# Performance work log

Hardware: AMD Instinct MI355X
Metric: run time of the kernel (lower is better)

Reference implementation:

```python
import jax, jax.numpy as jnp
import numpy as np

ALPHA = 0.2   # LeakyReLU negative slope
RATIO = 0.5   # blend ratio between attention and structural similarity
KHOP = 3      # k-hop structural similarity depth
NEG_BIG = -9e15


def _build_adj(edge, n):
    # edge: [N, D] int neighbor indices; adj[i, edge[i, d]] = 1
    rows = jnp.broadcast_to(jnp.arange(n)[:, None], edge.shape)
    return jnp.zeros((n, n), jnp.float32).at[rows, edge].set(1.0)


def _structural_similarity(adj, khop):
    # Sum of adjacency powers A + A^2 + ... + A^khop (k-hop reachability counts).
    s = adj
    p = adj
    for _ in range(khop - 1):
        p = p @ adj
        s = s + p
    return s


def _per_graph(atom, edge, W, a):
    n = atom.shape[0]
    adj = _build_adj(edge, n)
    structure = jax.nn.softmax(_structural_similarity(adj, KHOP), axis=1)
    h = atom @ W                                   # [N, F]
    f = h.shape[1]
    # a_input[i,j] = concat(h_i, h_j); a_input @ a == (h @ a1)_i + (h @ a2)_j
    src = h @ a[:f, 0]                             # [N]
    dst = h @ a[f:, 0]                             # [N]
    e = jax.nn.leaky_relu(src[:, None] + dst[None, :], ALPHA)  # [N, N]
    att = jnp.where(adj > 0, e, NEG_BIG)
    att = jax.nn.softmax(att, axis=1)
    blended = RATIO * att + (1.0 - RATIO) * structure
    return jax.nn.elu(blended @ h)                 # [N, F]


def setup_inputs() -> dict:
    key = jax.random.key(0)
    k1, k2, k3, k4 = jax.random.split(key, 4)
    B, N, D, F_IN, F_OUT = 16, 1024, 8, 128, 64
    atoms = jax.random.normal(k1, (B, N, F_IN), dtype=jnp.float32)
    edges = jax.random.randint(k2, (B, N, D), 0, N, dtype=jnp.int64)
    W = jax.random.normal(k3, (F_IN, F_OUT), dtype=jnp.float32) * 0.1
    a = jax.random.normal(k4, (2 * F_OUT, 1), dtype=jnp.float32) * 0.1
    return {"atoms": atoms, "edges": edges, "W": W, "a": a}


def reference(atoms, edges, W, a):
    return jax.vmap(_per_graph, in_axes=(0, 0, None, None))(atoms, edges, W, a)
```

## Files before the change

kernel.cpp:

```cpp
#include <hip/hip_runtime.h>

#define NN 1024
#define DG 8
#define FO 64
#define FI 128
#define LALPHA 0.2f
#define BR 16
#define SBS 257
#define MTS 1032

typedef __attribute__((ext_vector_type(8))) short bf16x8;
typedef __attribute__((ext_vector_type(4))) float f32x4;

static __device__ __forceinline__ unsigned short f2bf(float x) {
  union { float f; unsigned u; } v; v.f = x;
  unsigned r = v.u + 0x7FFFu + ((v.u >> 16) & 1u);
  return (unsigned short)(r >> 16);
}
static __device__ __forceinline__ float bf2f(unsigned short h) {
  union { unsigned u; float f; } v; v.u = ((unsigned)h) << 16;
  return v.f;
}

__global__ __launch_bounds__(256) void k_prep(const float* __restrict__ atoms,
                                              const float* __restrict__ W,
                                              const float* __restrict__ a,
                                              const int* __restrict__ edges,
                                              int* __restrict__ uniq,
                                              ushort* __restrict__ hT,
                                              float* __restrict__ srcv,
                                              float* __restrict__ dstv) {
  __shared__ float sp[16], dp[16];
  const int t = threadIdx.x, b = blockIdx.x;
  const int g = b >> 6;
  const int rbase = b * 16;

  if (t < 16) {
    sp[t] = 0.f; dp[t] = 0.f;
    const int rr = rbase + t;
    int e[DG];
#pragma unroll
    for (int s = 0; s < DG; s++) e[s] = edges[rr * DG + s];
#pragma unroll
    for (int s = 0; s < DG; s++) {
      int v = e[s];
      bool dup = false;
#pragma unroll
      for (int q = 0; q < DG; q++)
        if (q < s && e[q] == v) dup = true;
      uniq[rr * DG + s] = dup ? -1 : v;
    }
  }

  const int w = t >> 6, lane = t & 63, quad = lane >> 4, l16 = lane & 15;
  const float* __restrict__ Ar = atoms + (size_t)(rbase + l16) * FI;
  const float* __restrict__ Wc = W + w * 16 + l16;
  f32x4 acc = {0.f, 0.f, 0.f, 0.f};
#pragma unroll
  for (int kc = 0; kc < 4; kc++) {
    const int k0 = kc * 32 + quad * 8;
    float4 a0 = *(const float4*)(Ar + k0);
    float4 a1 = *(const float4*)(Ar + k0 + 4);
    float av[8] = {a0.x, a0.y, a0.z, a0.w, a1.x, a1.y, a1.z, a1.w};
    float wv[8];
#pragma unroll
    for (int e = 0; e < 8; e++) wv[e] = Wc[(k0 + e) * FO];
    bf16x8 ahi, alo, bhi, blo;
#pragma unroll
    for (int e = 0; e < 8; e++) {
      ushort h = f2bf(av[e]);
      ahi[e] = (short)h;
      alo[e] = (short)f2bf(av[e] - bf2f(h));
      ushort g2 = f2bf(wv[e]);
      bhi[e] = (short)g2;
      blo[e] = (short)f2bf(wv[e] - bf2f(g2));
    }
    acc = __builtin_amdgcn_mfma_f32_16x16x32_bf16(ahi, bhi, acc, 0, 0, 0);
    acc = __builtin_amdgcn_mfma_f32_16x16x32_bf16(ahi, blo, acc, 0, 0, 0);
    acc = __builtin_amdgcn_mfma_f32_16x16x32_bf16(alo, bhi, acc, 0, 0, 0);
  }

  const int f = w * 16 + l16;
  const float as_ = a[f], ad_ = a[FO + f];
  float ps[4], pd[4];
#pragma unroll
  for (int r = 0; r < 4; r++) {
    float v = acc[r];
    int rb = rbase + quad * 4 + r;
    hT[((size_t)g * FO + f) * NN + (rb & (NN - 1))] = f2bf(v);
    ps[r] = v * as_;
    pd[r] = v * ad_;
  }
#pragma unroll
  for (int off = 1; off < 16; off <<= 1)
#pragma unroll
    for (int r = 0; r < 4; r++) {
      ps[r] += __shfl_xor(ps[r], off);
      pd[r] += __shfl_xor(pd[r], off);
    }
  __syncthreads();
  if (l16 == 0) {
#pragma unroll
    for (int r = 0; r < 4; r++) {
      atomicAdd(&sp[quad * 4 + r], ps[r]);
      atomicAdd(&dp[quad * 4 + r], pd[r]);
    }
  }
  __syncthreads();
  if (t < 16) {
    srcv[rbase + t] = sp[t];
    dstv[rbase + t] = dp[t];
  }
}

__global__ __launch_bounds__(256) void k_fused(const int* __restrict__ uniq,
                                               const float* __restrict__ srcv,
                                               const float* __restrict__ dstv,
                                               const ushort* __restrict__ hT,
                                               float* __restrict__ out) {
  __shared__ unsigned Sb[BR * SBS];
  __shared__ __align__(16) ushort Mt[BR * MTS];
  __shared__ int n1[BR][DG];
  __shared__ float attw[BR][DG];
  __shared__ float zl[BR][16];
  __shared__ float Zr[BR];

  const int t = threadIdx.x, b = blockIdx.x;
  const int g = b >> 6, rbase = (b & 63) * BR;
  const int* __restrict__ Ug = uniq + (size_t)g * NN * DG;

  for (int i = t; i < BR * SBS; i += 256) Sb[i] = 0u;
  if (t < BR * DG) n1[t >> 3][t & 7] = Ug[(rbase + (t >> 3)) * DG + (t & 7)];
  __syncthreads();

  if (t < 128) {
    int r = t >> 3, s = t & 7;
    int j = n1[r][s];
    if (j >= 0) {
      atomicAdd(&Sb[r * SBS + (j >> 2)], 1u << ((j & 3) * 8));
      int4 k0 = *(const int4*)(Ug + j * DG);
      int4 k1 = *(const int4*)(Ug + j * DG + 4);
      int kk[8] = {k0.x, k0.y, k0.z, k0.w, k1.x, k1.y, k1.z, k1.w};
#pragma unroll
      for (int e = 0; e < 8; e++)
        if (kk[e] >= 0) atomicAdd(&Sb[r * SBS + (kk[e] >> 2)], 1u << ((kk[e] & 3) * 8));
    }
  } else if (t < 128 + BR) {
    int r = t - 128;
    float si = srcv[g * NN + rbase + r];
    float ev[DG];
    float m = -1e30f;
#pragma unroll
    for (int s = 0; s < DG; s++) {
      int j = n1[r][s];
      if (j >= 0) {
        float x = si + dstv[g * NN + j];
        x = x > 0.f ? x : LALPHA * x;
        ev[s] = x;
        m = fmaxf(m, x);
      } else ev[s] = -1e30f;
    }
    float sm = 0.f;
#pragma unroll
    for (int s = 0; s < DG; s++) {
      float e = (n1[r][s] >= 0) ? __expf(ev[s] - m) : 0.f;
      ev[s] = e;
      sm += e;
    }
    float inv = 1.f / sm;
#pragma unroll
    for (int s = 0; s < DG; s++) attw[r][s] = ev[s] * inv;
  }
#pragma unroll
  for (int q = 0; q < 4; q++) {
    int idx = t + 256 * q;
    int r = idx >> 6, e = idx & 63;
    int j = n1[r][e >> 3];
    if (j >= 0) {
      int k = Ug[j * DG + (e & 7)];
      if (k >= 0) {
        int4 m0 = *(const int4*)(Ug + k * DG);
        int4 m1 = *(const int4*)(Ug + k * DG + 4);
        int ll[8] = {m0.x, m0.y, m0.z, m0.w, m1.x, m1.y, m1.z, m1.w};
#pragma unroll
        for (int e2 = 0; e2 < 8; e2++)
          if (ll[e2] >= 0) atomicAdd(&Sb[r * SBS + (ll[e2] >> 2)], 1u << ((ll[e2] & 3) * 8));
      }
    }
  }
  __syncthreads();

  {
    const int r = t & 15, u = t >> 4;
    float zp = 0.f;
#pragma unroll
    for (int q = 0; q < 8; q++) {
      unsigned s0 = Sb[r * SBS + u * 16 + 2 * q];
      unsigned s1 = Sb[r * SBS + u * 16 + 2 * q + 1];
      float e0 = __expf((float)(s0 & 255u));
      float e1 = __expf((float)((s0 >> 8) & 255u));
      float e2 = __expf((float)((s0 >> 16) & 255u));
      float e3 = __expf((float)(s0 >> 24));
      float e4 = __expf((float)(s1 & 255u));
      float e5 = __expf((float)((s1 >> 8) & 255u));
      float e6 = __expf((float)((s1 >> 16) & 255u));
      float e7 = __expf((float)(s1 >> 24));
      zp += (e0 + e1) + (e2 + e3) + (e4 + e5) + (e6 + e7);
      union { uint4 v; ushort us[8]; } pk;
      pk.us[0] = f2bf(e0); pk.us[1] = f2bf(e1); pk.us[2] = f2bf(e2); pk.us[3] = f2bf(e3);
      pk.us[4] = f2bf(e4); pk.us[5] = f2bf(e5); pk.us[6] = f2bf(e6); pk.us[7] = f2bf(e7);
      *(uint4*)&Mt[r * MTS + u * 64 + q * 8] = pk.v;
    }
    zl[r][u] = zp;
  }
  __syncthreads();

  if (t < 128) {
    const int r = t >> 3, s = t & 7;
    float z = 0.f;
#pragma unroll
    for (int u = 0; u < 16; u++) z += zl[r][u];
    if (s == 0) Zr[r] = z;
    int j = n1[r][s];
    if (j >= 0) {
      int adr = r * MTS + j;
      Mt[adr] = f2bf(bf2f(Mt[adr]) + attw[r][s] * z);
    }
  }
  __syncthreads();

  const int w = t >> 6, lane = t & 63, quad = lane >> 4, l16 = lane & 15;
  const ushort* __restrict__ hrow = hT + ((size_t)g * FO + w * 16 + l16) * NN;
  f32x4 acc = {0.f, 0.f, 0.f, 0.f};
#pragma unroll 8
  for (int ks = 0; ks < NN; ks += 32) {
    bf16x8 af = *(const bf16x8*)&Mt[l16 * MTS + ks + quad * 8];
    bf16x8 bf = *(const bf16x8*)(hrow + ks + quad * 8);
    acc = __builtin_amdgcn_mfma_f32_16x16x32_bf16(af, bf, acc, 0, 0, 0);
  }
#pragma unroll
  for (int r = 0; r < 4; r++) {
    int rl = quad * 4 + r;
    float v = acc[r] * (0.5f / Zr[rl]);
    v = v > 0.f ? v : __expf(v) - 1.f;
    out[((size_t)(g * NN + rbase + rl)) * FO + w * 16 + l16] = v;
  }
}

extern "C" void kernel_launch(void* const* d_in, const int* in_sizes, int n_in,
                              void* d_out, int out_size, void* d_ws, size_t ws_size,
                              hipStream_t stream) {
  const float* atoms = (const float*)d_in[0];
  const int* edges = (const int*)d_in[1];
  const float* W = (const float*)d_in[2];
  const float* a = (const float*)d_in[3];
  float* out = (float*)d_out;

  const int nrows = in_sizes[0] / FI;
  const int ngraph = nrows / NN;

  ushort* hT = (ushort*)d_ws;
  float* srcv = (float*)(hT + (size_t)ngraph * FO * NN);
  float* dstv = srcv + nrows;
  int* uniq = (int*)(dstv + nrows);

  k_prep<<<nrows / 16, 256, 0, stream>>>(atoms, W, a, edges, uniq, hT, srcv, dstv);
  k_fused<<<ngraph * (NN / BR), 256, 0, stream>>>(uniq, srcv, dstv, hT, out);
}
```

Measured before the change: 101.5 us.

## Stage graph neighbor table in LDS and merge 2-hop/3-hop scatter loops

Each block now copies the whole per-graph uniq neighbor table (1024x8 ints, 32KB) into shared memory, aliased with the Mt buffer, before building the k-hop count matrix. Neighbor gathers for hops 2 and 3 then read from LDS instead of scattered global/L2 loads. The hop-1 and hop-2 atomic updates are folded into the same loop that handles hop 3, so all 256 threads share the work instead of only half of them. The cost is an extra 32KB global read per block (1024 blocks) and a reshaped shared-memory layout, which may lower occupancy.

```diff
diff --git a/kernel.cpp b/kernel.cpp
--- a/kernel.cpp
+++ b/kernel.cpp
@@ -113,40 +113,64 @@
   }
 }
 
+#define SM_MT    0
+#define SM_SB    33024
+#define SM_N1    (33024 + 16448)
+#define SM_ATT   (SM_N1 + 512)
+#define SM_ZL    (SM_ATT + 512)
+#define SM_ZR    (SM_ZL + 1024)
+#define SM_TOT   (SM_ZR + 64)
+
 __global__ __launch_bounds__(256) void k_fused(const int* __restrict__ uniq,
                                                const float* __restrict__ srcv,
                                                const float* __restrict__ dstv,
                                                const ushort* __restrict__ hT,
                                                float* __restrict__ out) {
-  __shared__ unsigned Sb[BR * SBS];
-  __shared__ __align__(16) ushort Mt[BR * MTS];
-  __shared__ int n1[BR][DG];
-  __shared__ float attw[BR][DG];
-  __shared__ float zl[BR][16];
-  __shared__ float Zr[BR];
+  __shared__ __align__(16) unsigned char SM[SM_TOT];
+  int* __restrict__ Us = (int*)SM;
+  ushort* __restrict__ Mt = (ushort*)SM;
+  unsigned* __restrict__ Sb = (unsigned*)(SM + SM_SB);
+  int(*n1)[DG] = (int(*)[DG])(SM + SM_N1);
+  float(*attw)[DG] = (float(*)[DG])(SM + SM_ATT);
+  float(*zl)[16] = (float(*)[16])(SM + SM_ZL);
+  float* Zr = (float*)(SM + SM_ZR);
 
   const int t = threadIdx.x, b = blockIdx.x;
   const int g = b >> 6, rbase = (b & 63) * BR;
   const int* __restrict__ Ug = uniq + (size_t)g * NN * DG;
 
+  {
+    const int4* Ug4 = (const int4*)Ug;
+    int4* Us4 = (int4*)Us;
+#pragma unroll
+    for (int q = 0; q < 8; q++) Us4[t + 256 * q] = Ug4[t + 256 * q];
+  }
   for (int i = t; i < BR * SBS; i += 256) Sb[i] = 0u;
   if (t < BR * DG) n1[t >> 3][t & 7] = Ug[(rbase + (t >> 3)) * DG + (t & 7)];
   __syncthreads();
 
-  if (t < 128) {
-    int r = t >> 3, s = t & 7;
-    int j = n1[r][s];
+#pragma unroll
+  for (int q = 0; q < 4; q++) {
+    int idx = t + 256 * q;
+    int r = idx >> 6, e = idx & 63;
+    int j = n1[r][e >> 3];
     if (j >= 0) {
-      atomicAdd(&Sb[r * SBS + (j >> 2)], 1u << ((j & 3) * 8));
-      int4 k0 = *(const int4*)(Ug + j * DG);
-      int4 k1 = *(const int4*)(Ug + j * DG + 4);
-      int kk[8] = {k0.x, k0.y, k0.z, k0.w, k1.x, k1.y, k1.z, k1.w};
-#pragma unroll
-      for (int e = 0; e < 8; e++)
-        if (kk[e] >= 0) atomicAdd(&Sb[r * SBS + (kk[e] >> 2)], 1u << ((kk[e] & 3) * 8));
-    }
-  } else if (t < 128 + BR) {
-    int r = t - 128;
+      if ((e & 7) == 0)
+        atomicAdd(&Sb[r * SBS + (j >> 2)], 1u << ((j & 3) * 8));
+      int k = Us[j * DG + (e & 7)];
+      if (k >= 0) {
+        atomicAdd(&Sb[r * SBS + (k >> 2)], 1u << ((k & 3) * 8));
+        int4 m0 = *(const int4*)(Us + k * DG);
+        int4 m1 = *(const int4*)(Us + k * DG + 4);
+        int ll[8] = {m0.x, m0.y, m0.z, m0.w, m1.x, m1.y, m1.z, m1.w};
+#pragma unroll
+        for (int e2 = 0; e2 < 8; e2++)
+          if (ll[e2] >= 0) atomicAdd(&Sb[r * SBS + (ll[e2] >> 2)], 1u << ((ll[e2] & 3) * 8));
+      }
+    }
+  }
+  if (t < BR) {
+    int r = t;
     float si = srcv[g * NN + rbase + r];
     float ev[DG];
     float m = -1e30f;
@@ -170,23 +194,6 @@
     float inv = 1.f / sm;
 #pragma unroll
     for (int s = 0; s < DG; s++) attw[r][s] = ev[s] * inv;
-  }
-#pragma unroll
-  for (int q = 0; q < 4; q++) {
-    int idx = t + 256 * q;
-    int r = idx >> 6, e = idx & 63;
-    int j = n1[r][e >> 3];
-    if (j >= 0) {
-      int k = Ug[j * DG + (e & 7)];
-      if (k >= 0) {
-        int4 m0 = *(const int4*)(Ug + k * DG);
-        int4 m1 = *(const int4*)(Ug + k * DG + 4);
-        int ll[8] = {m0.x, m0.y, m0.z, m0.w, m1.x, m1.y, m1.z, m1.w};
-#pragma unroll
-        for (int e2 = 0; e2 < 8; e2++)
-          if (ll[e2] >= 0) atomicAdd(&Sb[r * SBS + (ll[e2] >> 2)], 1u << ((ll[e2] & 3) * 8));
-      }
-    }
   }
   __syncthreads();
 
```

Result: no change. 101.5 us (+0.0%).

## Compute structure exp inline in MFMA loop and apply sparse attention separately

Applied to the files above, without the earlier changes.

Drops the 32KB bf16 Mt staging matrix. The exp of the k-hop counts is now computed directly from the packed Sb counters inside the MFMA loop, and the row sums are reduced with shuffles. The sparse attention term is applied as a separate gather over a new row-major h copy (hN) written by k_prep, instead of being folded into the dense matrix. The one-hop and two-hop atomics are merged into one 4-pass loop and occupancy is hinted at 6 blocks per CU. The aim is to cut LDS use and barriers, at the cost of redundant exp work per wave (each of 4 waves recomputes the same A-fragments) and an extra global write in prep.

```diff
diff --git a/kernel.cpp b/kernel.cpp
--- a/kernel.cpp
+++ b/kernel.cpp
@@ -7,7 +7,7 @@
 #define LALPHA 0.2f
 #define BR 16
 #define SBS 257
-#define MTS 1032
+#define AHS 68
 
 typedef __attribute__((ext_vector_type(8))) short bf16x8;
 typedef __attribute__((ext_vector_type(4))) float f32x4;
@@ -28,6 +28,7 @@
                                               const int* __restrict__ edges,
                                               int* __restrict__ uniq,
                                               ushort* __restrict__ hT,
+                                              ushort* __restrict__ hN,
                                               float* __restrict__ srcv,
                                               float* __restrict__ dstv) {
   __shared__ float sp[16], dp[16];
@@ -87,7 +88,9 @@
   for (int r = 0; r < 4; r++) {
     float v = acc[r];
     int rb = rbase + quad * 4 + r;
-    hT[((size_t)g * FO + f) * NN + (rb & (NN - 1))] = f2bf(v);
+    ushort hv = f2bf(v);
+    hT[((size_t)g * FO + f) * NN + (rb & (NN - 1))] = hv;
+    hN[(size_t)rb * FO + f] = hv;
     ps[r] = v * as_;
     pd[r] = v * ad_;
   }
@@ -113,17 +116,16 @@
   }
 }
 
-__global__ __launch_bounds__(256) void k_fused(const int* __restrict__ uniq,
-                                               const float* __restrict__ srcv,
-                                               const float* __restrict__ dstv,
-                                               const ushort* __restrict__ hT,
-                                               float* __restrict__ out) {
+__global__ __launch_bounds__(256, 6) void k_fused(const int* __restrict__ uniq,
+                                                  const float* __restrict__ srcv,
+                                                  const float* __restrict__ dstv,
+                                                  const ushort* __restrict__ hT,
+                                                  const ushort* __restrict__ hN,
+                                                  float* __restrict__ out) {
   __shared__ unsigned Sb[BR * SBS];
-  __shared__ __align__(16) ushort Mt[BR * MTS];
+  __shared__ float attH[BR * AHS];
   __shared__ int n1[BR][DG];
   __shared__ float attw[BR][DG];
-  __shared__ float zl[BR][16];
-  __shared__ float Zr[BR];
 
   const int t = threadIdx.x, b = blockIdx.x;
   const int g = b >> 6, rbase = (b & 63) * BR;
@@ -133,20 +135,28 @@
   if (t < BR * DG) n1[t >> 3][t & 7] = Ug[(rbase + (t >> 3)) * DG + (t & 7)];
   __syncthreads();
 
-  if (t < 128) {
-    int r = t >> 3, s = t & 7;
-    int j = n1[r][s];
+#pragma unroll
+  for (int q = 0; q < 4; q++) {
+    int idx = t + 256 * q;
+    int r = idx >> 6, e = idx & 63;
+    int j = n1[r][e >> 3];
     if (j >= 0) {
-      atomicAdd(&Sb[r * SBS + (j >> 2)], 1u << ((j & 3) * 8));
-      int4 k0 = *(const int4*)(Ug + j * DG);
-      int4 k1 = *(const int4*)(Ug + j * DG + 4);
-      int kk[8] = {k0.x, k0.y, k0.z, k0.w, k1.x, k1.y, k1.z, k1.w};
-#pragma unroll
-      for (int e = 0; e < 8; e++)
-        if (kk[e] >= 0) atomicAdd(&Sb[r * SBS + (kk[e] >> 2)], 1u << ((kk[e] & 3) * 8));
-    }
-  } else if (t < 128 + BR) {
-    int r = t - 128;
+      if ((e & 7) == 0)
+        atomicAdd(&Sb[r * SBS + (j >> 2)], 1u << ((j & 3) * 8));
+      int k = Ug[j * DG + (e & 7)];
+      if (k >= 0) {
+        atomicAdd(&Sb[r * SBS + (k >> 2)], 1u << ((k & 3) * 8));
+        int4 m0 = *(const int4*)(Ug + k * DG);
+        int4 m1 = *(const int4*)(Ug + k * DG + 4);
+        int ll[8] = {m0.x, m0.y, m0.z, m0.w, m1.x, m1.y, m1.z, m1.w};
+#pragma unroll
+        for (int e2 = 0; e2 < 8; e2++)
+          if (ll[e2] >= 0) atomicAdd(&Sb[r * SBS + (ll[e2] >> 2)], 1u << ((ll[e2] & 3) * 8));
+      }
+    }
+  }
+  if (t < BR) {
+    int r = t;
     float si = srcv[g * NN + rbase + r];
     float ev[DG];
     float m = -1e30f;
@@ -171,79 +181,66 @@
 #pragma unroll
     for (int s = 0; s < DG; s++) attw[r][s] = ev[s] * inv;
   }
-#pragma unroll
-  for (int q = 0; q < 4; q++) {
-    int idx = t + 256 * q;
-    int r = idx >> 6, e = idx & 63;
-    int j = n1[r][e >> 3];
-    if (j >= 0) {
-      int k = Ug[j * DG + (e & 7)];
-      if (k >= 0) {
-        int4 m0 = *(const int4*)(Ug + k * DG);
-        int4 m1 = *(const int4*)(Ug + k * DG + 4);
-        int ll[8] = {m0.x, m0.y, m0.z, m0.w, m1.x, m1.y, m1.z, m1.w};
-#pragma unroll
-        for (int e2 = 0; e2 < 8; e2++)
-          if (ll[e2] >= 0) atomicAdd(&Sb[r * SBS + (ll[e2] >> 2)], 1u << ((ll[e2] & 3) * 8));
+  __syncthreads();
+
+  {
+    const int r = t >> 4, f0 = (t & 15) * 4;
+    float a0 = 0.f, a1 = 0.f, a2 = 0.f, a3 = 0.f;
+#pragma unroll
+    for (int s = 0; s < DG; s++) {
+      int j = n1[r][s];
+      if (j >= 0) {
+        float wgt = attw[r][s];
+        uint2 hv = *(const uint2*)(hN + ((size_t)(g * NN + j)) * FO + f0);
+        a0 += wgt * bf2f((ushort)(hv.x & 0xffffu));
+        a1 += wgt * bf2f((ushort)(hv.x >> 16));
+        a2 += wgt * bf2f((ushort)(hv.y & 0xffffu));
+        a3 += wgt * bf2f((ushort)(hv.y >> 16));
       }
     }
-  }
-  __syncthreads();
-
-  {
-    const int r = t & 15, u = t >> 4;
-    float zp = 0.f;
-#pragma unroll
-    for (int q = 0; q < 8; q++) {
-      unsigned s0 = Sb[r * SBS + u * 16 + 2 * q];
-      unsigned s1 = Sb[r * SBS + u * 16 + 2 * q + 1];
-      float e0 = __expf((float)(s0 & 255u));
-      float e1 = __expf((float)((s0 >> 8) & 255u));
-      float e2 = __expf((float)((s0 >> 16) & 255u));
-      float e3 = __expf((float)(s0 >> 24));
-      float e4 = __expf((float)(s1 & 255u));
-      float e5 = __expf((float)((s1 >> 8) & 255u));
-      float e6 = __expf((float)((s1 >> 16) & 255u));
-      float e7 = __expf((float)(s1 >> 24));
-      zp += (e0 + e1) + (e2 + e3) + (e4 + e5) + (e6 + e7);
-      union { uint4 v; ushort us[8]; } pk;
-      pk.us[0] = f2bf(e0); pk.us[1] = f2bf(e1); pk.us[2] = f2bf(e2); pk.us[3] = f2bf(e3);
-      pk.us[4] = f2bf(e4); pk.us[5] = f2bf(e5); pk.us[6] = f2bf(e6); pk.us[7] = f2bf(e7);
-      *(uint4*)&Mt[r * MTS + u * 64 + q * 8] = pk.v;
-    }
-    zl[r][u] = zp;
-  }
-  __syncthreads();
-
-  if (t < 128) {
-    const int r = t >> 3, s = t & 7;
-    float z = 0.f;
-#pragma unroll
-    for (int u = 0; u < 16; u++) z += zl[r][u];
-    if (s == 0) Zr[r] = z;
-    int j = n1[r][s];
-    if (j >= 0) {
-      int adr = r * MTS + j;
-      Mt[adr] = f2bf(bf2f(Mt[adr]) + attw[r][s] * z);
-    }
+    attH[r * AHS + f0] = a0;
+    attH[r * AHS + f0 + 1] = a1;
+    attH[r * AHS + f0 + 2] = a2;
+    attH[r * AHS + f0 + 3] = a3;
   }
   __syncthreads();
 
   const int w = t >> 6, lane = t & 63, quad = lane >> 4, l16 = lane & 15;
   const ushort* __restrict__ hrow = hT + ((size_t)g * FO + w * 16 + l16) * NN;
   f32x4 acc = {0.f, 0.f, 0.f, 0.f};
+  float zacc = 0.f;
 #pragma unroll 8
   for (int ks = 0; ks < NN; ks += 32) {
-    bf16x8 af = *(const bf16x8*)&Mt[l16 * MTS + ks + quad * 8];
+    const int wd = l16 * SBS + (ks >> 2) + quad * 2;
+    unsigned s0 = Sb[wd], s1 = Sb[wd + 1];
+    float e0 = __expf((float)(s0 & 255u));
+    float e1 = __expf((float)((s0 >> 8) & 255u));
+    float e2 = __expf((float)((s0 >> 16) & 255u));
+    float e3 = __expf((float)(s0 >> 24));
+    float e4 = __expf((float)(s1 & 255u));
+    float e5 = __expf((float)((s1 >> 8) & 255u));
+    float e6 = __expf((float)((s1 >> 16) & 255u));
+    float e7 = __expf((float)(s1 >> 24));
+    zacc += (e0 + e1) + (e2 + e3) + (e4 + e5) + (e6 + e7);
+    bf16x8 af;
+    af[0] = (short)f2bf(e0); af[1] = (short)f2bf(e1);
+    af[2] = (short)f2bf(e2); af[3] = (short)f2bf(e3);
+    af[4] = (short)f2bf(e4); af[5] = (short)f2bf(e5);
+    af[6] = (short)f2bf(e6); af[7] = (short)f2bf(e7);
     bf16x8 bf = *(const bf16x8*)(hrow + ks + quad * 8);
     acc = __builtin_amdgcn_mfma_f32_16x16x32_bf16(af, bf, acc, 0, 0, 0);
   }
+  zacc += __shfl_xor(zacc, 16);
+  zacc += __shfl_xor(zacc, 32);
+
 #pragma unroll
   for (int r = 0; r < 4; r++) {
-    int rl = quad * 4 + r;
-    float v = acc[r] * (0.5f / Zr[rl]);
+    const int row = quad * 4 + r;
+    float Z = __shfl(zacc, row);
+    float att = attH[row * AHS + w * 16 + l16];
+    float v = 0.5f * att + acc[r] * (0.5f / Z);
     v = v > 0.f ? v : __expf(v) - 1.f;
-    out[((size_t)(g * NN + rbase + rl)) * FO + w * 16 + l16] = v;
+    out[((size_t)(g * NN + rbase + row)) * FO + w * 16 + l16] = v;
   }
 }
 
@@ -260,10 +257,11 @@
   const int ngraph = nrows / NN;
 
   ushort* hT = (ushort*)d_ws;
-  float* srcv = (float*)(hT + (size_t)ngraph * FO * NN);
+  ushort* hN = hT + (size_t)ngraph * FO * NN;
+  float* srcv = (float*)(hN + (size_t)nrows * FO);
   float* dstv = srcv + nrows;
   int* uniq = (int*)(dstv + nrows);
 
-  k_prep<<<nrows / 16, 256, 0, stream>>>(atoms, W, a, edges, uniq, hT, srcv, dstv);
-  k_fused<<<ngraph * (NN / BR), 256, 0, stream>>>(uniq, srcv, dstv, hT, out);
-}
+  k_prep<<<nrows / 16, 256, 0, stream>>>(atoms, W, a, edges, uniq, hT, hN, srcv, dstv);
+  k_fused<<<ngraph * (NN / BR), 256, 0, stream>>>(uniq, srcv, dstv, hT, hN, out);
+}
```

Result: faster. 98.01 us (-3.4%).
